# Performance work log

Measured on AMD Instinct MI355X. Metric: run time of the kernel, lower is better.

## Reference

```python
import jax, jax.numpy as jnp
import numpy as np

D = 64
FACTOR = 4
HID = D * FACTOR  # 256
BATCH = 262144


def _ancestors(adj):
    # boolean transitive closure: reach[j, i] True if j is an ancestor of i
    reach = adj.copy()
    for _ in range(adj.shape[0]):
        reach = reach | ((reach.astype(np.int32) @ adj.astype(np.int32)) > 0)
    return reach


def _build_mask():
    rng = np.random.RandomState(0)
    adj = np.triu(rng.rand(D, D) < 0.3, k=1)  # adj[j, i]: j is a parent of i (DAG)
    A = _ancestors(adj)
    B = A.copy()
    B[np.eye(D, dtype=bool)] = True  # B = self.B in the torch module
    return B


def setup_inputs() -> dict:
    key = jax.random.key(0)
    ks = jax.random.split(key, 10)
    Bmask = _build_mask()
    s_in = 1.0 / np.sqrt(D)
    s_hid = 1.0 / np.sqrt(HID)
    return {
        "x": jax.random.normal(ks[0], (BATCH, D), dtype=jnp.float32),
        "eps": jax.random.normal(ks[1], (BATCH, D), dtype=jnp.float32),
        "enc1_w": jax.random.normal(ks[2], (D, HID), dtype=jnp.float32) * s_in,
        "enc1_b": jnp.zeros((HID,), dtype=jnp.float32),
        "enc3_w": jax.random.normal(ks[3], (HID, 2 * D), dtype=jnp.float32) * s_hid,
        "enc3_b": jnp.zeros((2 * D,), dtype=jnp.float32),
        # per-node decoder weights, zero-padded to full input dim D;
        # node i only reads inputs j where Bmask[j, i] is True
        "dec1_w": jax.random.normal(ks[4], (D, D, HID), dtype=jnp.float32) * s_in,
        "dec1_b": jnp.zeros((D, HID), dtype=jnp.float32),
        "dec3_w": jax.random.normal(ks[5], (D, HID), dtype=jnp.float32) * s_hid,
        "dec3_b": jnp.zeros((D,), dtype=jnp.float32),
        "B_mask": jnp.asarray(Bmask, dtype=jnp.bool_),  # [in_node j, node i]
    }


def reference(x, eps, enc1_w, enc1_b, enc3_w, enc3_b,
              dec1_w, dec1_b, dec3_w, dec3_b, B_mask):
    d = D
    # ---- encoder ----
    h = jax.nn.relu(x @ enc1_w + enc1_b)          # [B, HID]
    z = h @ enc3_w + enc3_b                        # [B, 2d]
    zz = z.reshape(-1, 2, d)
    mu = zz[:, 0, :]                               # [B, d]
    log_var = zz[:, 1, :]                          # [B, d]
    # reparameterize (rsample with externally supplied standard normal eps)
    eps_y = mu + jnp.exp(log_var * 0.5) * eps      # [B, d]
    # ---- per-node decoder ----
    # mask_in[i, j] = B_mask[j, i]: which input latents node i gathers.
    mask_in = B_mask.T.astype(dec1_w.dtype)        # [node, in]
    W1 = dec1_w * mask_in[:, :, None]              # zero out non-ancestor inputs
    outs = []
    for i in range(d):  # d structurally distinct tiny MLPs (static loop)
        hi = jax.nn.relu(eps_y @ W1[i] + dec1_b[i])   # [B, HID]
        outs.append(hi @ dec3_w[i] + dec3_b[i])       # [B]
    x_out = jnp.stack(outs, axis=1)                # [B, d] (no_noise=True path)
    # y_recon in torch is zeros_like(enc3 output): [B, 2d], second half untouched
    y_recon = jnp.concatenate([x_out, jnp.zeros_like(x_out)], axis=1)
    return (x_out, mu, log_var, y_recon)
```

## Files before the change

kernel.cpp:

```cpp
#include <hip/hip_runtime.h>
#include <hip/hip_bf16.h>

#define BATCH_N 262144

typedef __attribute__((ext_vector_type(8))) __bf16 bf16x8;
typedef __attribute__((ext_vector_type(4))) float f32x4;
typedef __attribute__((ext_vector_type(2))) float f32x2;

#define OFF_EPSY  0UL
#define OFF_W1T   33554432UL
#define OFF_BW    35651584UL
#define OFF_E1HI  35782656UL
#define OFF_E1LO  35815424UL
#define OFF_E3HI  35848192UL
#define OFF_E3LO  35913728UL
#define OFF_NQ    35979264UL
#define OFF_CMASK 35979520UL

__device__ __forceinline__ void split_f32(float v, __bf16& hi, __bf16& lo) {
    __bf16 h = (__bf16)v;
    hi = h;
    lo = (__bf16)(v - (float)h);
}

__global__ __launch_bounds__(256) void cvae_prep0(
    const unsigned char* __restrict__ bm, char* __restrict__ ws)
{
    __shared__ int diag_ok;
    int t = threadIdx.x;
    if (t == 0) diag_ok = 1;
    __syncthreads();
    if (t < 64) { if (bm[t * 65] == 0) atomicAnd(&diag_ok, 0); }
    __syncthreads();
    int isbool = diag_ok;
    unsigned char* cm = (unsigned char*)(ws + OFF_CMASK);
    for (int idx = t; idx < 4096; idx += 256) {
        unsigned char v;
        if (isbool) v = bm[idx] ? 1 : 0;
        else        v = ((const unsigned int*)bm)[idx] ? 1 : 0;
        cm[idx] = v;
    }
}

__global__ __launch_bounds__(256) void cvae_prep(
    const float* __restrict__ enc1_w, const float* __restrict__ enc3_w,
    const float* __restrict__ dec1_w, const float* __restrict__ dec1_b,
    const float* __restrict__ dec3_w, char* __restrict__ ws)
{
    const int bid = blockIdx.x, tid = threadIdx.x;
    const unsigned char* cm = (const unsigned char*)(ws + OFF_CMASK);
    if (bid < 8) {
        int g = bid * 256 + tid;
        int j = g >> 3, kc = (g & 7) * 8;
        __bf16* e1hi = (__bf16*)(ws + OFF_E1HI);
        __bf16* e1lo = (__bf16*)(ws + OFF_E1LO);
        bf16x8 vh, vl;
        #pragma unroll
        for (int e = 0; e < 8; ++e) {
            __bf16 h, l;
            split_f32(enc1_w[(kc + e) * 256 + j], h, l);
            vh[e] = h; vl[e] = l;
        }
        *(bf16x8*)(e1hi + j * 64 + kc) = vh;
        *(bf16x8*)(e1lo + j * 64 + kc) = vl;
    } else if (bid < 24) {
        int g = (bid - 8) * 256 + tid;
        int j = g >> 5, kc = (g & 31) * 8;
        __bf16* e3hi = (__bf16*)(ws + OFF_E3HI);
        __bf16* e3lo = (__bf16*)(ws + OFF_E3LO);
        bf16x8 vh, vl;
        #pragma unroll
        for (int e = 0; e < 8; ++e) {
            __bf16 h, l;
            split_f32(enc3_w[(kc + e) * 128 + j], h, l);
            vh[e] = h; vl[e] = l;
        }
        *(bf16x8*)(e3hi + j * 256 + kc) = vh;
        *(bf16x8*)(e3lo + j * 256 + kc) = vl;
    } else if (bid < 536) {
        int g = (bid - 24) * 256 + tid;
        int i = g >> 11;
        int rem = g & 2047;
        int j = rem >> 3, kc = (rem & 7) * 8;
        __bf16* w1t = (__bf16*)(ws + OFF_W1T);
        bf16x8 v;
        #pragma unroll
        for (int e = 0; e < 8; ++e) {
            int k = kc + e;
            float m = cm[k * 64 + i] ? 1.0f : 0.0f;
            v[e] = (__bf16)(dec1_w[(i * 64 + k) * 256 + j] * m);
        }
        *(bf16x8*)(w1t + ((size_t)(i * 256 + j)) * 64 + kc) = v;
    } else if (bid < 600) {
        int g = (bid - 536) * 256 + tid;
        float2* bw = (float2*)(ws + OFF_BW);
        float2 p; p.x = dec1_b[g]; p.y = dec3_w[g];
        bw[g] = p;
    } else {
        if (tid < 64) {
            int any = 0;
            for (int k = 32; k < 64; ++k) any |= (int)cm[k * 64 + tid];
            ((int*)(ws + OFF_NQ))[tid] = any ? 2 : 1;
        }
    }
}

__global__ __launch_bounds__(256, 2) void cvae_encoder(
    const float* __restrict__ x, const float* __restrict__ eps,
    const float* __restrict__ enc1_b, const float* __restrict__ enc3_b,
    float* __restrict__ out, char* __restrict__ ws)
{
    __shared__ float hbuf[16384];
    const int tid = threadIdx.x;
    const int w = tid >> 6, l = tid & 63;
    const int lr = l & 15, lg = l >> 4;
    const size_t rowbase = (size_t)blockIdx.x * 64 + w * 16;
    const size_t arow = rowbase + lr;

    const __bf16* e1hi = (const __bf16*)(ws + OFF_E1HI);
    const __bf16* e1lo = (const __bf16*)(ws + OFF_E1LO);
    const __bf16* e3hi = (const __bf16*)(ws + OFF_E3HI);
    const __bf16* e3lo = (const __bf16*)(ws + OFF_E3LO);
    __bf16* epsy = (__bf16*)(ws + OFF_EPSY);
    float* muo = out + (size_t)BATCH_N * 64;
    float* lvo = out + (size_t)BATCH_N * 128;

    bf16x8 xhi[2], xlo[2];
    #pragma unroll
    for (int q = 0; q < 2; ++q) {
        const float* xp = x + arow * 64 + q * 32 + lg * 8;
        #pragma unroll
        for (int e = 0; e < 8; ++e) {
            __bf16 h, lo2; split_f32(xp[e], h, lo2);
            xhi[q][e] = h; xlo[q][e] = lo2;
        }
    }
    float* hw = hbuf + w * 4096;

    for (int t = 0; t < 16; ++t) {
        int j = t * 16 + lr;
        bf16x8 bh0 = *(const bf16x8*)(e1hi + j * 64 + lg * 8);
        bf16x8 bh1 = *(const bf16x8*)(e1hi + j * 64 + 32 + lg * 8);
        bf16x8 bl0 = *(const bf16x8*)(e1lo + j * 64 + lg * 8);
        bf16x8 bl1 = *(const bf16x8*)(e1lo + j * 64 + 32 + lg * 8);
        float b = enc1_b[j];
        f32x4 acc = {b, b, b, b};
        acc = __builtin_amdgcn_mfma_f32_16x16x32_bf16(xhi[0], bh0, acc, 0, 0, 0);
        acc = __builtin_amdgcn_mfma_f32_16x16x32_bf16(xhi[1], bh1, acc, 0, 0, 0);
        acc = __builtin_amdgcn_mfma_f32_16x16x32_bf16(xlo[0], bh0, acc, 0, 0, 0);
        acc = __builtin_amdgcn_mfma_f32_16x16x32_bf16(xlo[1], bh1, acc, 0, 0, 0);
        acc = __builtin_amdgcn_mfma_f32_16x16x32_bf16(xhi[0], bl0, acc, 0, 0, 0);
        acc = __builtin_amdgcn_mfma_f32_16x16x32_bf16(xhi[1], bl1, acc, 0, 0, 0);
        #pragma unroll
        for (int e = 0; e < 4; ++e) {
            int wr = lg * 4 + e;
            hw[(wr * 256 + j) ^ ((wr & 7) << 2)] = fmaxf(acc[e], 0.0f);
        }
    }

    bf16x8 hhi[8], hlo[8];
    #pragma unroll
    for (int q = 0; q < 8; ++q) {
        int k0 = q * 32 + lg * 8;
        int w0 = (lr * 256 + k0) ^ ((lr & 7) << 2);
        int w1 = (lr * 256 + k0 + 4) ^ ((lr & 7) << 2);
        f32x4 a = *(const f32x4*)(hw + w0);
        f32x4 c = *(const f32x4*)(hw + w1);
        #pragma unroll
        for (int e = 0; e < 4; ++e) {
            __bf16 h, lo2;
            split_f32(a[e], h, lo2); hhi[q][e] = h;     hlo[q][e] = lo2;
            split_f32(c[e], h, lo2); hhi[q][4 + e] = h; hlo[q][4 + e] = lo2;
        }
    }

    f32x4 macc[4];
    #pragma unroll
    for (int t2 = 0; t2 < 8; ++t2) {
        int j2 = t2 * 16 + lr;
        float b2 = enc3_b[j2];
        f32x4 acc = {b2, b2, b2, b2};
        #pragma unroll
        for (int q = 0; q < 8; ++q) {
            bf16x8 bh = *(const bf16x8*)(e3hi + j2 * 256 + q * 32 + lg * 8);
            bf16x8 bl = *(const bf16x8*)(e3lo + j2 * 256 + q * 32 + lg * 8);
            acc = __builtin_amdgcn_mfma_f32_16x16x32_bf16(hhi[q], bh, acc, 0, 0, 0);
            acc = __builtin_amdgcn_mfma_f32_16x16x32_bf16(hlo[q], bh, acc, 0, 0, 0);
            acc = __builtin_amdgcn_mfma_f32_16x16x32_bf16(hhi[q], bl, acc, 0, 0, 0);
        }
        if (t2 < 4) {
            macc[t2] = acc;
            #pragma unroll
            for (int e = 0; e < 4; ++e)
                muo[(rowbase + lg * 4 + e) * 64 + j2] = acc[e];
        } else {
            int jm = j2 - 64;
            #pragma unroll
            for (int e = 0; e < 4; ++e) {
                size_t r = rowbase + lg * 4 + e;
                float lv = acc[e];
                lvo[r * 64 + jm] = lv;
                float ey = macc[t2 - 4][e] +
                           exp2f(lv * 0.72134752044448170f) * eps[r * 64 + jm];
                epsy[r * 64 + jm] = (__bf16)ey;
            }
        }
    }
}

template<int NQ>
__device__ __forceinline__ void dec_accum(
    const __bf16* __restrict__ wp, const float2* __restrict__ bwp,
    const bf16x8 (&af)[8][2], f32x2 (&ps)[8][2])
{
    bf16x8 pb0[3], pb1[3];
    float2 pbw[3];
    #pragma unroll
    for (int s = 0; s < 2; ++s) {
        pb0[s] = *(const bf16x8*)(wp + (size_t)s * 1024);
        if (NQ == 2) pb1[s] = *(const bf16x8*)(wp + (size_t)s * 1024 + 32);
        else         pb1[s] = pb0[s];
        pbw[s] = bwp[s * 16];
    }
    pb0[2] = pb0[0]; pb1[2] = pb1[0]; pbw[2] = pbw[0];

    #pragma unroll
    for (int t = 0; t < 16; ++t) {
        const int cur = t % 3;
        const int nxt = (t + 2) % 3;
        if (t + 2 < 16) {
            pb0[nxt] = *(const bf16x8*)(wp + (size_t)(t + 2) * 1024);
            if (NQ == 2) pb1[nxt] = *(const bf16x8*)(wp + (size_t)(t + 2) * 1024 + 32);
            pbw[nxt] = bwp[(t + 2) * 16];
        }
        float2 bwv = pbw[cur];
        f32x4 bias = {bwv.x, bwv.x, bwv.x, bwv.x};
        f32x2 wv; wv[0] = bwv.y; wv[1] = bwv.y;
        #pragma unroll
        for (int r = 0; r < 8; ++r) {
            f32x4 acc = __builtin_amdgcn_mfma_f32_16x16x32_bf16(af[r][0], pb0[cur], bias, 0, 0, 0);
            if (NQ == 2)
                acc = __builtin_amdgcn_mfma_f32_16x16x32_bf16(af[r][1], pb1[cur], acc, 0, 0, 0);
            f32x2 p0, p1;
            p0[0] = fmaxf(acc[0], 0.f); p0[1] = fmaxf(acc[1], 0.f);
            p1[0] = fmaxf(acc[2], 0.f); p1[1] = fmaxf(acc[3], 0.f);
            asm("v_pk_fma_f32 %0, %1, %2, %0" : "+v"(ps[r][0]) : "v"(p0), "v"(wv));
            asm("v_pk_fma_f32 %0, %1, %2, %0" : "+v"(ps[r][1]) : "v"(p1), "v"(wv));
        }
    }
}

__global__ __launch_bounds__(256, 2) void cvae_decoder(
    const char* __restrict__ ws, const float* __restrict__ dec3_b,
    float* __restrict__ out)
{
    __shared__ float xt[128 * 68];
    const int tid = threadIdx.x;
    const int w = tid >> 6, l = tid & 63;
    const int lr = l & 15, lg = l >> 4;
    const size_t rb = (size_t)blockIdx.x * 128;
    const __bf16* epsy = (const __bf16*)(ws + OFF_EPSY);
    const __bf16* w1t  = (const __bf16*)(ws + OFF_W1T);
    const float2* bw   = (const float2*)(ws + OFF_BW);
    const int* nqt     = (const int*)(ws + OFF_NQ);

    bf16x8 af[8][2];
    #pragma unroll
    for (int r = 0; r < 8; ++r)
        #pragma unroll
        for (int q = 0; q < 2; ++q)
            af[r][q] = *(const bf16x8*)(epsy + (rb + r * 16 + lr) * 64 + q * 32 + lg * 8);

    for (int ii = 0; ii < 16; ++ii) {
        const int i = ii * 4 + w;
        const __bf16* wp = w1t + ((size_t)i * 256 + lr) * 64 + lg * 8;
        const float2* bwp = bw + i * 256 + lr;
        f32x2 ps[8][2];
        #pragma unroll
        for (int r = 0; r < 8; ++r) {
            ps[r][0] = (f32x2){0.f, 0.f};
            ps[r][1] = (f32x2){0.f, 0.f};
        }
        if (nqt[i] == 2) dec_accum<2>(wp, bwp, af, ps);
        else             dec_accum<1>(wp, bwp, af, ps);

        const float b3 = dec3_b[i];
        float pv[8][4];
        #pragma unroll
        for (int r = 0; r < 8; ++r) {
            pv[r][0] = ps[r][0][0]; pv[r][1] = ps[r][0][1];
            pv[r][2] = ps[r][1][0]; pv[r][3] = ps[r][1][1];
        }
        #pragma unroll
        for (int r = 0; r < 8; ++r)
            #pragma unroll
            for (int e = 0; e < 4; ++e) {
                float v = pv[r][e];
                v += __shfl_xor(v, 1);
                v += __shfl_xor(v, 2);
                v += __shfl_xor(v, 4);
                v += __shfl_xor(v, 8);
                pv[r][e] = v + b3;
            }
        if (lr == (i & 15)) {
            #pragma unroll
            for (int r = 0; r < 8; ++r)
                #pragma unroll
                for (int e = 0; e < 4; ++e)
                    xt[(r * 16 + lg * 4 + e) * 68 + i] = pv[r][e];
        }
    }
    __syncthreads();

    float* yr = out + (size_t)BATCH_N * 192;
    #pragma unroll
    for (int c = 0; c < 8; ++c) {
        int idx = c * 1024 + tid * 4;
        int row = idx >> 6, col = idx & 63;
        f32x4 v = *(const f32x4*)(xt + row * 68 + col);
        *(f32x4*)(out + (rb + row) * 64 + col) = v;
        *(f32x4*)(yr + (rb + row) * 128 + col) = v;
        f32x4 z = {0.f, 0.f, 0.f, 0.f};
        *(f32x4*)(yr + (rb + row) * 128 + 64 + col) = z;
    }
}

extern "C" void kernel_launch(void* const* d_in, const int* in_sizes, int n_in,
                              void* d_out, int out_size, void* d_ws, size_t ws_size,
                              hipStream_t stream)
{
    (void)in_sizes; (void)n_in; (void)out_size; (void)ws_size;
    const float* x      = (const float*)d_in[0];
    const float* eps    = (const float*)d_in[1];
    const float* enc1_w = (const float*)d_in[2];
    const float* enc1_b = (const float*)d_in[3];
    const float* enc3_w = (const float*)d_in[4];
    const float* enc3_b = (const float*)d_in[5];
    const float* dec1_w = (const float*)d_in[6];
    const float* dec1_b = (const float*)d_in[7];
    const float* dec3_w = (const float*)d_in[8];
    const float* dec3_b = (const float*)d_in[9];
    const unsigned char* bmask = (const unsigned char*)d_in[10];
    float* out = (float*)d_out;
    char* ws = (char*)d_ws;

    hipLaunchKernelGGL(cvae_prep0, dim3(1), dim3(256), 0, stream, bmask, ws);
    hipLaunchKernelGGL(cvae_prep, dim3(601), dim3(256), 0, stream,
                       enc1_w, enc3_w, dec1_w, dec1_b, dec3_w, ws);
    hipLaunchKernelGGL(cvae_encoder, dim3(BATCH_N / 64), dim3(256), 0, stream,
                       x, eps, enc1_b, enc3_b, out, ws);
    hipLaunchKernelGGL(cvae_decoder, dim3(BATCH_N / 128), dim3(256), 0, stream,
                       ws, dec3_b, out);
}
```

Measured before the change: 990.2 us.

## Split encoder hidden layer into halves and shrink decoder row tile for occupancy

The encoder now computes the hidden layer in two 128-column halves and accumulates the second GEMM across halves. This halves the shared-memory staging buffer and the per-thread hi/lo register fragments. The decoder processes 64 rows per block instead of 128, which halves the activation fragments and accumulators. Both kernels raise launch bounds to target 4 blocks per SM. The trade-off is that each decoder block re-reads all per-node weights for fewer rows, which doubles weight traffic per row.

```diff
diff --git a/kernel.cpp b/kernel.cpp
--- a/kernel.cpp
+++ b/kernel.cpp
@@ -105,12 +105,12 @@
     }
 }
 
-__global__ __launch_bounds__(256, 2) void cvae_encoder(
+__global__ __launch_bounds__(256, 4) void cvae_encoder(
     const float* __restrict__ x, const float* __restrict__ eps,
     const float* __restrict__ enc1_b, const float* __restrict__ enc3_b,
     float* __restrict__ out, char* __restrict__ ws)
 {
-    __shared__ float hbuf[16384];
+    __shared__ float hbuf[8192];
     const int tid = threadIdx.x;
     const int w = tid >> 6, l = tid & 63;
     const int lr = l & 15, lg = l >> 4;
@@ -135,75 +135,91 @@
             xhi[q][e] = h; xlo[q][e] = lo2;
         }
     }
-    float* hw = hbuf + w * 4096;
-
-    for (int t = 0; t < 16; ++t) {
-        int j = t * 16 + lr;
-        bf16x8 bh0 = *(const bf16x8*)(e1hi + j * 64 + lg * 8);
-        bf16x8 bh1 = *(const bf16x8*)(e1hi + j * 64 + 32 + lg * 8);
-        bf16x8 bl0 = *(const bf16x8*)(e1lo + j * 64 + lg * 8);
-        bf16x8 bl1 = *(const bf16x8*)(e1lo + j * 64 + 32 + lg * 8);
-        float b = enc1_b[j];
-        f32x4 acc = {b, b, b, b};
-        acc = __builtin_amdgcn_mfma_f32_16x16x32_bf16(xhi[0], bh0, acc, 0, 0, 0);
-        acc = __builtin_amdgcn_mfma_f32_16x16x32_bf16(xhi[1], bh1, acc, 0, 0, 0);
-        acc = __builtin_amdgcn_mfma_f32_16x16x32_bf16(xlo[0], bh0, acc, 0, 0, 0);
-        acc = __builtin_amdgcn_mfma_f32_16x16x32_bf16(xlo[1], bh1, acc, 0, 0, 0);
-        acc = __builtin_amdgcn_mfma_f32_16x16x32_bf16(xhi[0], bl0, acc, 0, 0, 0);
-        acc = __builtin_amdgcn_mfma_f32_16x16x32_bf16(xhi[1], bl1, acc, 0, 0, 0);
+    float* hw = hbuf + w * 2048;
+
+    f32x4 acc2[8];
+    #pragma unroll
+    for (int t2 = 0; t2 < 8; ++t2) {
+        float b2 = enc3_b[t2 * 16 + lr];
+        acc2[t2] = (f32x4){b2, b2, b2, b2};
+    }
+
+    #pragma unroll
+    for (int half = 0; half < 2; ++half) {
+        #pragma unroll
+        for (int t = 0; t < 8; ++t) {
+            int j = half * 128 + t * 16 + lr;
+            bf16x8 bh0 = *(const bf16x8*)(e1hi + j * 64 + lg * 8);
+            bf16x8 bh1 = *(const bf16x8*)(e1hi + j * 64 + 32 + lg * 8);
+            bf16x8 bl0 = *(const bf16x8*)(e1lo + j * 64 + lg * 8);
+            bf16x8 bl1 = *(const bf16x8*)(e1lo + j * 64 + 32 + lg * 8);
+            float b = enc1_b[j];
+            f32x4 acc = {b, b, b, b};
+            acc = __builtin_amdgcn_mfma_f32_16x16x32_bf16(xhi[0], bh0, acc, 0, 0, 0);
+            acc = __builtin_amdgcn_mfma_f32_16x16x32_bf16(xhi[1], bh1, acc, 0, 0, 0);
+            acc = __builtin_amdgcn_mfma_f32_16x16x32_bf16(xlo[0], bh0, acc, 0, 0, 0);
+            acc = __builtin_amdgcn_mfma_f32_16x16x32_bf16(xlo[1], bh1, acc, 0, 0, 0);
+            acc = __builtin_amdgcn_mfma_f32_16x16x32_bf16(xhi[0], bl0, acc, 0, 0, 0);
+            acc = __builtin_amdgcn_mfma_f32_16x16x32_bf16(xhi[1], bl1, acc, 0, 0, 0);
+            int jj = t * 16 + lr;
+            #pragma unroll
+            for (int e = 0; e < 4; ++e) {
+                int wr = lg * 4 + e;
+                hw[(wr * 128 + jj) ^ ((wr & 7) << 2)] = fmaxf(acc[e], 0.0f);
+            }
+        }
+
+        bf16x8 hhi[4], hlo[4];
+        #pragma unroll
+        for (int qq = 0; qq < 4; ++qq) {
+            int k0 = qq * 32 + lg * 8;
+            int w0 = (lr * 128 + k0) ^ ((lr & 7) << 2);
+            int w1 = (lr * 128 + k0 + 4) ^ ((lr & 7) << 2);
+            f32x4 a = *(const f32x4*)(hw + w0);
+            f32x4 c = *(const f32x4*)(hw + w1);
+            #pragma unroll
+            for (int e = 0; e < 4; ++e) {
+                __bf16 h, lo2;
+                split_f32(a[e], h, lo2); hhi[qq][e] = h;     hlo[qq][e] = lo2;
+                split_f32(c[e], h, lo2); hhi[qq][4 + e] = h; hlo[qq][4 + e] = lo2;
+            }
+        }
+
+        #pragma unroll
+        for (int t2 = 0; t2 < 8; ++t2) {
+            int j2 = t2 * 16 + lr;
+            f32x4 acc = acc2[t2];
+            #pragma unroll
+            for (int qq = 0; qq < 4; ++qq) {
+                int q = half * 4 + qq;
+                bf16x8 bh = *(const bf16x8*)(e3hi + j2 * 256 + q * 32 + lg * 8);
+                bf16x8 bl = *(const bf16x8*)(e3lo + j2 * 256 + q * 32 + lg * 8);
+                acc = __builtin_amdgcn_mfma_f32_16x16x32_bf16(hhi[qq], bh, acc, 0, 0, 0);
+                acc = __builtin_amdgcn_mfma_f32_16x16x32_bf16(hlo[qq], bh, acc, 0, 0, 0);
+                acc = __builtin_amdgcn_mfma_f32_16x16x32_bf16(hhi[qq], bl, acc, 0, 0, 0);
+            }
+            acc2[t2] = acc;
+        }
+    }
+
+    #pragma unroll
+    for (int t2 = 0; t2 < 4; ++t2) {
+        int j2 = t2 * 16 + lr;
+        #pragma unroll
+        for (int e = 0; e < 4; ++e)
+            muo[(rowbase + lg * 4 + e) * 64 + j2] = acc2[t2][e];
+    }
+    #pragma unroll
+    for (int t2 = 4; t2 < 8; ++t2) {
+        int jm = t2 * 16 + lr - 64;
         #pragma unroll
         for (int e = 0; e < 4; ++e) {
-            int wr = lg * 4 + e;
-            hw[(wr * 256 + j) ^ ((wr & 7) << 2)] = fmaxf(acc[e], 0.0f);
-        }
-    }
-
-    bf16x8 hhi[8], hlo[8];
-    #pragma unroll
-    for (int q = 0; q < 8; ++q) {
-        int k0 = q * 32 + lg * 8;
-        int w0 = (lr * 256 + k0) ^ ((lr & 7) << 2);
-        int w1 = (lr * 256 + k0 + 4) ^ ((lr & 7) << 2);
-        f32x4 a = *(const f32x4*)(hw + w0);
-        f32x4 c = *(const f32x4*)(hw + w1);
-        #pragma unroll
-        for (int e = 0; e < 4; ++e) {
-            __bf16 h, lo2;
-            split_f32(a[e], h, lo2); hhi[q][e] = h;     hlo[q][e] = lo2;
-            split_f32(c[e], h, lo2); hhi[q][4 + e] = h; hlo[q][4 + e] = lo2;
-        }
-    }
-
-    f32x4 macc[4];
-    #pragma unroll
-    for (int t2 = 0; t2 < 8; ++t2) {
-        int j2 = t2 * 16 + lr;
-        float b2 = enc3_b[j2];
-        f32x4 acc = {b2, b2, b2, b2};
-        #pragma unroll
-        for (int q = 0; q < 8; ++q) {
-            bf16x8 bh = *(const bf16x8*)(e3hi + j2 * 256 + q * 32 + lg * 8);
-            bf16x8 bl = *(const bf16x8*)(e3lo + j2 * 256 + q * 32 + lg * 8);
-            acc = __builtin_amdgcn_mfma_f32_16x16x32_bf16(hhi[q], bh, acc, 0, 0, 0);
-            acc = __builtin_amdgcn_mfma_f32_16x16x32_bf16(hlo[q], bh, acc, 0, 0, 0);
-            acc = __builtin_amdgcn_mfma_f32_16x16x32_bf16(hhi[q], bl, acc, 0, 0, 0);
-        }
-        if (t2 < 4) {
-            macc[t2] = acc;
-            #pragma unroll
-            for (int e = 0; e < 4; ++e)
-                muo[(rowbase + lg * 4 + e) * 64 + j2] = acc[e];
-        } else {
-            int jm = j2 - 64;
-            #pragma unroll
-            for (int e = 0; e < 4; ++e) {
-                size_t r = rowbase + lg * 4 + e;
-                float lv = acc[e];
-                lvo[r * 64 + jm] = lv;
-                float ey = macc[t2 - 4][e] +
-                           exp2f(lv * 0.72134752044448170f) * eps[r * 64 + jm];
-                epsy[r * 64 + jm] = (__bf16)ey;
-            }
+            size_t r = rowbase + lg * 4 + e;
+            float lv = acc2[t2][e];
+            lvo[r * 64 + jm] = lv;
+            float ey = acc2[t2 - 4][e] +
+                       exp2f(lv * 0.72134752044448170f) * eps[r * 64 + jm];
+            epsy[r * 64 + jm] = (__bf16)ey;
         }
     }
 }
@@ -211,7 +227,7 @@
 template<int NQ>
 __device__ __forceinline__ void dec_accum(
     const __bf16* __restrict__ wp, const float2* __restrict__ bwp,
-    const bf16x8 (&af)[8][2], f32x2 (&ps)[8][2])
+    const bf16x8 (&af)[4][2], f32x2 (&ps)[4][2])
 {
     bf16x8 pb0[3], pb1[3];
     float2 pbw[3];
@@ -237,7 +253,7 @@
         f32x4 bias = {bwv.x, bwv.x, bwv.x, bwv.x};
         f32x2 wv; wv[0] = bwv.y; wv[1] = bwv.y;
         #pragma unroll
-        for (int r = 0; r < 8; ++r) {
+        for (int r = 0; r < 4; ++r) {
             f32x4 acc = __builtin_amdgcn_mfma_f32_16x16x32_bf16(af[r][0], pb0[cur], bias, 0, 0, 0);
             if (NQ == 2)
                 acc = __builtin_amdgcn_mfma_f32_16x16x32_bf16(af[r][1], pb1[cur], acc, 0, 0, 0);
@@ -250,23 +266,23 @@
     }
 }
 
-__global__ __launch_bounds__(256, 2) void cvae_decoder(
+__global__ __launch_bounds__(256, 4) void cvae_decoder(
     const char* __restrict__ ws, const float* __restrict__ dec3_b,
     float* __restrict__ out)
 {
-    __shared__ float xt[128 * 68];
+    __shared__ float xt[64 * 68];
     const int tid = threadIdx.x;
     const int w = tid >> 6, l = tid & 63;
     const int lr = l & 15, lg = l >> 4;
-    const size_t rb = (size_t)blockIdx.x * 128;
+    const size_t rb = (size_t)blockIdx.x * 64;
     const __bf16* epsy = (const __bf16*)(ws + OFF_EPSY);
     const __bf16* w1t  = (const __bf16*)(ws + OFF_W1T);
     const float2* bw   = (const float2*)(ws + OFF_BW);
     const int* nqt     = (const int*)(ws + OFF_NQ);
 
-    bf16x8 af[8][2];
-    #pragma unroll
-    for (int r = 0; r < 8; ++r)
+    bf16x8 af[4][2];
+    #pragma unroll
+    for (int r = 0; r < 4; ++r)
         #pragma unroll
         for (int q = 0; q < 2; ++q)
             af[r][q] = *(const bf16x8*)(epsy + (rb + r * 16 + lr) * 64 + q * 32 + lg * 8);
@@ -275,9 +291,9 @@
         const int i = ii * 4 + w;
         const __bf16* wp = w1t + ((size_t)i * 256 + lr) * 64 + lg * 8;
         const float2* bwp = bw + i * 256 + lr;
-        f32x2 ps[8][2];
-        #pragma unroll
-        for (int r = 0; r < 8; ++r) {
+        f32x2 ps[4][2];
+        #pragma unroll
+        for (int r = 0; r < 4; ++r) {
             ps[r][0] = (f32x2){0.f, 0.f};
             ps[r][1] = (f32x2){0.f, 0.f};
         }
@@ -285,14 +301,14 @@
         else             dec_accum<1>(wp, bwp, af, ps);
 
         const float b3 = dec3_b[i];
-        float pv[8][4];
-        #pragma unroll
-        for (int r = 0; r < 8; ++r) {
+        float pv[4][4];
+        #pragma unroll
+        for (int r = 0; r < 4; ++r) {
             pv[r][0] = ps[r][0][0]; pv[r][1] = ps[r][0][1];
             pv[r][2] = ps[r][1][0]; pv[r][3] = ps[r][1][1];
         }
         #pragma unroll
-        for (int r = 0; r < 8; ++r)
+        for (int r = 0; r < 4; ++r)
             #pragma unroll
             for (int e = 0; e < 4; ++e) {
                 float v = pv[r][e];
@@ -304,7 +320,7 @@
             }
         if (lr == (i & 15)) {
             #pragma unroll
-            for (int r = 0; r < 8; ++r)
+            for (int r = 0; r < 4; ++r)
                 #pragma unroll
                 for (int e = 0; e < 4; ++e)
                     xt[(r * 16 + lg * 4 + e) * 68 + i] = pv[r][e];
@@ -314,7 +330,7 @@
 
     float* yr = out + (size_t)BATCH_N * 192;
     #pragma unroll
-    for (int c = 0; c < 8; ++c) {
+    for (int c = 0; c < 4; ++c) {
         int idx = c * 1024 + tid * 4;
         int row = idx >> 6, col = idx & 63;
         f32x4 v = *(const f32x4*)(xt + row * 68 + col);
@@ -349,6 +365,6 @@
                        enc1_w, enc3_w, dec1_w, dec1_b, dec3_w, ws);
     hipLaunchKernelGGL(cvae_encoder, dim3(BATCH_N / 64), dim3(256), 0, stream,
                        x, eps, enc1_b, enc3_b, out, ws);
-    hipLaunchKernelGGL(cvae_decoder, dim3(BATCH_N / 128), dim3(256), 0, stream,
+    hipLaunchKernelGGL(cvae_decoder, dim3(BATCH_N / 64), dim3(256), 0, stream,
                        ws, dec3_b, out);
 }
```

Measured after the change: 1.286 ms. 1.3x slower.
